# Optimization experiments

Measured on AMD Instinct MI355X. Metric: run time of the kernel, lower is better.

The kernel has to match this reference:

```python
import jax, jax.numpy as jnp
import numpy as np

N_NODES = 50000
N_EDGES = 800000
IN_CH = 128
HID = 32
HEADS = 8
OUT_CH = 40
NEG_SLOPE = 0.2


def setup_inputs() -> dict:
    key = jax.random.key(0)
    ks = jax.random.split(key, 12)
    g = lambda k, shape, fan: (jax.random.normal(k, shape, jnp.float32) / np.sqrt(fan).astype(np.float32))
    return {
        "x": jax.random.normal(ks[0], (N_NODES, IN_CH), jnp.float32),
        "edge_index": jax.random.randint(ks[1], (2, N_EDGES), 0, N_NODES, jnp.int64),
        "W1l": g(ks[2], (IN_CH, HEADS * HID), IN_CH),
        "W1r": g(ks[3], (IN_CH, HEADS * HID), IN_CH),
        "att1": g(ks[4], (HEADS, HID), HID),
        "b1": jnp.zeros((HEADS * HID,), jnp.float32),
        "W2l": g(ks[5], (HEADS * HID, HID), HEADS * HID),
        "W2r": g(ks[6], (HEADS * HID, HID), HEADS * HID),
        "att2": g(ks[7], (1, HID), HID),
        "b2": jnp.zeros((HID,), jnp.float32),
        "Wc": g(ks[8], (HID + IN_CH, OUT_CH), HID + IN_CH),
        "bc": jnp.zeros((OUT_CH,), jnp.float32),
    }


def _gatv2(x, ei, Wl, Wr, att, b, heads, ch):
    # GATv2Conv (concat=True): e_ij = att . LeakyReLU(Wl x_j + Wr x_i)
    n = x.shape[0]
    src, dst = ei[0], ei[1]  # message flows src(j) -> dst(i)
    xl = (x @ Wl).reshape(n, heads, ch)  # source transform
    xr = (x @ Wr).reshape(n, heads, ch)  # target transform
    e = jax.nn.leaky_relu(xl[src] + xr[dst], NEG_SLOPE)  # [E, H, C]
    score = jnp.einsum("ehc,hc->eh", e, att)             # [E, H]
    # per-target-node segment softmax (stable)
    m = jax.ops.segment_max(score, dst, num_segments=n)
    alpha = jnp.exp(score - m[dst])
    denom = jax.ops.segment_sum(alpha, dst, num_segments=n)
    alpha = alpha / denom[dst]
    out = jax.ops.segment_sum(alpha[:, :, None] * xl[src], dst, num_segments=n)
    return out.reshape(n, heads * ch) + b


def reference(x, edge_index, W1l, W1r, att1, b1, W2l, W2r, att2, b2, Wc, bc):
    n = x.shape[0]
    ar = jnp.arange(n, dtype=edge_index.dtype)
    ei = jnp.concatenate([edge_index, jnp.stack([ar, ar])], axis=1)  # add self-loops
    h1 = jax.nn.elu(_gatv2(x, ei, W1l, W1r, att1, b1, HEADS, HID))
    h2 = jax.nn.elu(_gatv2(h1, ei, W2l, W2r, att2, b2, 1, HID))
    combined = jnp.concatenate([h2, x], axis=1)
    return combined @ Wc + bc
```

## Files before the change

### kernel.cpp

```cpp
#include <hip/hip_runtime.h>
#include <cstdint>
#include <cstddef>
#include <math.h>

#define NN 50000
#define INCH 128
#define HIDC 32
#define NHEAD 8
#define OUTC 40

typedef unsigned short ushort_t;
using bf16x8 = __attribute__((ext_vector_type(8))) short;
using f32x4  = __attribute__((ext_vector_type(4))) float;

__device__ __forceinline__ float bf2f(unsigned short h) {
    return __uint_as_float(((unsigned int)h) << 16);
}
__device__ __forceinline__ unsigned short f2bf(float f) {
    unsigned int u = __float_as_uint(f);
    u = u + 0x7FFFu + ((u >> 16) & 1u);
    return (unsigned short)(u >> 16);
}
__device__ __forceinline__ float lo16(unsigned int u) { return __uint_as_float(u << 16); }
__device__ __forceinline__ float hi16(unsigned int u) { return __uint_as_float(u & 0xffff0000u); }

__global__ __launch_bounds__(256) void prep_all(
    const float* __restrict__ x, ushort_t* __restrict__ xb, int total8,
    const float* __restrict__ W1l, const float* __restrict__ W1r,
    const float* __restrict__ W2l, const float* __restrict__ W2r,
    const float* __restrict__ Wc,
    ushort_t* __restrict__ BT1, ushort_t* __restrict__ BT2, ushort_t* __restrict__ BTc,
    const int* __restrict__ ei, int E, int n, int* __restrict__ deg, int CX) {
    const int blk = blockIdx.x;
    const int tid = threadIdx.x;
    if (blk < CX) {
        int i = blk * 256 + tid;
        if (i >= total8) return;
        float4 f0 = *(const float4*)(x + (size_t)i * 8);
        float4 f1 = *(const float4*)(x + (size_t)i * 8 + 4);
        ushort4 u0, u1;
        u0.x = f2bf(f0.x); u0.y = f2bf(f0.y); u0.z = f2bf(f0.z); u0.w = f2bf(f0.w);
        u1.x = f2bf(f1.x); u1.y = f2bf(f1.y); u1.z = f2bf(f1.z); u1.w = f2bf(f1.w);
        *(ushort4*)(xb + (size_t)i * 8) = u0;
        *(ushort4*)(xb + (size_t)i * 8 + 4) = u1;
    } else if (blk < CX + 616) {
        int b = blk - CX, k = tid;
        if (b < 512) {
            if (k < 128) {
                float v = (b < 256) ? W1l[(size_t)k * 256 + b] : W1r[(size_t)k * 256 + (b - 256)];
                BT1[(size_t)b * 128 + k] = f2bf(v);
            }
        } else if (b < 576) {
            int c = b - 512;
            float v = (c < 32) ? W2l[(size_t)k * 32 + c] : W2r[(size_t)k * 32 + (c - 32)];
            BT2[(size_t)c * 256 + k] = f2bf(v);
        } else {
            int c = b - 576;
            if (k < 160) BTc[(size_t)c * 160 + k] = f2bf(Wc[(size_t)k * 40 + c]);
        }
    } else {
        int e = (blk - CX - 616) * 256 + tid;
        if (e >= E + n) return;
        int dst = (e < E) ? ei[E + e] : (e - E);
        atomicAdd(&deg[dst], 1);
    }
}


__global__ __launch_bounds__(1024) void partial_scan(
    const int* __restrict__ deg, int* __restrict__ row_start,
    int* __restrict__ block_total, int n) {
    __shared__ int wsum[16];
    const int tid = threadIdx.x, lane = tid & 63, wid = tid >> 6;
    int i = blockIdx.x * 1024 + tid;
    int v = (i < n) ? deg[i] : 0;
    int s = v;
    #pragma unroll
    for (int off = 1; off < 64; off <<= 1) {
        int t = __shfl_up(s, off, 64);
        if (lane >= off) s += t;
    }
    if (lane == 63) wsum[wid] = s;
    __syncthreads();
    if (wid == 0) {
        int ws = (lane < 16) ? wsum[lane] : 0;
        #pragma unroll
        for (int off = 1; off < 16; off <<= 1) {
            int t = __shfl_up(ws, off, 64);
            if (lane >= off) ws += t;
        }
        if (lane < 16) wsum[lane] = ws;
    }
    __syncthreads();
    int wexcl = wid ? wsum[wid - 1] : 0;
    if (i < n) row_start[i] = wexcl + s - v;
    if (tid == 0) block_total[blockIdx.x] = wsum[15];
}

__global__ void totals_scan(const int* __restrict__ block_total, int* __restrict__ block_off,
                            int* __restrict__ row_start_n, int nb) {
    int j = threadIdx.x;
    int v = (j < nb) ? block_total[j] : 0;
    int s = v;
    #pragma unroll
    for (int off = 1; off < 64; off <<= 1) {
        int t = __shfl_up(s, off, 64);
        if (j >= off) s += t;
    }
    if (j < nb) block_off[j] = s - v;
    if (j == nb - 1) *row_start_n = s;
}

__global__ __launch_bounds__(1024) void add_off(int* __restrict__ row_start, int* __restrict__ cursor,
                                                const int* __restrict__ block_off, int n) {
    int i = blockIdx.x * 1024 + threadIdx.x;
    if (i >= n) return;
    int val = row_start[i] + block_off[blockIdx.x];
    row_start[i] = val;
    cursor[i] = val;
}

__global__ void scatter_edges(const int* __restrict__ ei, int E, int n,
                              int* __restrict__ cursor, int* __restrict__ csr_src) {
    int e = blockIdx.x * blockDim.x + threadIdx.x;
    if (e >= E + n) return;
    int src, dst;
    if (e < E) { src = ei[e]; dst = ei[E + e]; } else { src = dst = e - E; }
    int pos = atomicAdd(&cursor[dst], 1);
    csr_src[pos] = src;
}

__global__ __launch_bounds__(256) void gemm1_mfma(
    const ushort_t* __restrict__ xb, const ushort_t* __restrict__ BT1,
    const float* __restrict__ att,
    ushort_t* __restrict__ xl1, ushort_t* __restrict__ xr1,
    float* __restrict__ dl, float* __restrict__ dr, int M) {
    __shared__ ushort_t As[128][72];
    __shared__ ushort_t Bs[128][72];
    const int tid = threadIdx.x;
    const int rowBase = blockIdx.y * 128;
    const int bx = blockIdx.x;
    const int c0 = bx * 128;
    const int wid = tid >> 6, lane = tid & 63;
    const int wr = wid >> 1, wc = wid & 1;
    const int l15 = lane & 15, l4 = lane >> 4;
    f32x4 acc[4][4];
    #pragma unroll
    for (int i = 0; i < 4; ++i)
        #pragma unroll
        for (int j = 0; j < 4; ++j)
            #pragma unroll
            for (int q = 0; q < 4; ++q) acc[i][j][q] = 0.f;

    for (int c = 0; c < 2; ++c) {
        #pragma unroll
        for (int h = 0; h < 4; ++h) {
            int idx = h * 256 + tid;
            int r = idx >> 3, seg = idx & 7;
            int row = rowBase + r;
            uint4 v = {0, 0, 0, 0};
            if (row < M) v = *(const uint4*)(xb + (size_t)row * 128 + c * 64 + seg * 8);
            *(uint4*)&As[r][seg * 8] = v;
            *(uint4*)&Bs[r][seg * 8] = *(const uint4*)(BT1 + (size_t)(c0 + r) * 128 + c * 64 + seg * 8);
        }
        __syncthreads();
        #pragma unroll
        for (int kk = 0; kk < 2; ++kk) {
            bf16x8 a[4], b[4];
            #pragma unroll
            for (int f = 0; f < 4; ++f) {
                a[f] = *(const bf16x8*)&As[wr * 64 + f * 16 + l15][kk * 32 + l4 * 8];
                b[f] = *(const bf16x8*)&Bs[wc * 64 + f * 16 + l15][kk * 32 + l4 * 8];
            }
            #pragma unroll
            for (int i = 0; i < 4; ++i)
                #pragma unroll
                for (int j = 0; j < 4; ++j)
                    acc[i][j] = __builtin_amdgcn_mfma_f32_16x16x32_bf16(a[i], b[j], acc[i][j], 0, 0, 0);
        }
        __syncthreads();
    }
    ushort_t* __restrict__ cout = (bx < 2) ? xl1 : xr1;
    const int colBase = (bx & 1) * 128;
    #pragma unroll
    for (int i = 0; i < 4; ++i)
        #pragma unroll
        for (int r = 0; r < 4; ++r) {
            int row = rowBase + wr * 64 + i * 16 + l4 * 4 + r;
            if (row >= M) continue;
            #pragma unroll
            for (int j = 0; j < 4; ++j) {
                int col = colBase + wc * 64 + j * 16 + l15;
                cout[(size_t)row * 256 + col] = f2bf(acc[i][j][r]);
            }
        }
    float attv[4];
    #pragma unroll
    for (int j = 0; j < 4; ++j)
        attv[j] = att[(bx & 1) * 128 + wc * 64 + j * 16 + l15];
    float* __restrict__ dst = (bx < 2) ? dl : dr;
    const int headA = (bx & 1) * 4 + wc * 2;
    #pragma unroll
    for (int i = 0; i < 4; ++i)
        #pragma unroll
        for (int r = 0; r < 4; ++r) {
            float s0 = fmaf(acc[i][1][r], attv[1], acc[i][0][r] * attv[0]);
            float s1 = fmaf(acc[i][3][r], attv[3], acc[i][2][r] * attv[2]);
            s0 += __shfl_xor(s0, 1); s1 += __shfl_xor(s1, 1);
            s0 += __shfl_xor(s0, 2); s1 += __shfl_xor(s1, 2);
            s0 += __shfl_xor(s0, 4); s1 += __shfl_xor(s1, 4);
            s0 += __shfl_xor(s0, 8); s1 += __shfl_xor(s1, 8);
            if (l15 == 0) {
                int row = rowBase + wr * 64 + i * 16 + l4 * 4 + r;
                if (row < M) {
                    dst[(size_t)row * 8 + headA] = s0;
                    dst[(size_t)row * 8 + headA + 1] = s1;
                }
            }
        }
}

__global__ __launch_bounds__(256) void gat_agg1(
    const ushort_t* __restrict__ xl, const ushort_t* __restrict__ xr,
    const float* __restrict__ dl, const float* __restrict__ dr,
    const float* __restrict__ att, const float* __restrict__ b,
    const int* __restrict__ row_start, const int* __restrict__ csr_src,
    ushort_t* __restrict__ h1) {
    const int lane = threadIdx.x & 63;
    const int i = blockIdx.x * 4 + (threadIdx.x >> 6);
    const int half = lane >> 5;
    const int sl = lane & 31;
    const int head = sl >> 2;

    uint4 xv = *(const uint4*)(xr + (size_t)i * 256 + sl * 8);
    const float xr0 = lo16(xv.x), xr1 = hi16(xv.x), xr2 = lo16(xv.y), xr3 = hi16(xv.y);
    const float xr4 = lo16(xv.z), xr5 = hi16(xv.z), xr6 = lo16(xv.w), xr7 = hi16(xv.w);
    const float4 atA = *(const float4*)(att + sl * 8);
    const float4 atB = *(const float4*)(att + sl * 8 + 4);
    const float cbase = 0.6f * dr[(size_t)i * 8 + head];
    const int p0 = row_start[i], p1 = row_start[i + 1];

    float d = 0.f;
    float a0 = 0.f, a1 = 0.f, a2 = 0.f, a3 = 0.f, a4 = 0.f, a5 = 0.f, a6 = 0.f, a7 = 0.f;

    int e0 = p0 + half;     int pc0 = e0 < p1 ? e0 : p1 - 1;
    int j0 = csr_src[pc0];
    uint4 uv0 = *(const uint4*)(xl + (size_t)j0 * 256 + sl * 8);
    float dl0 = dl[(size_t)j0 * 8 + head];
    int e1 = p0 + half + 2; int pc1 = e1 < p1 ? e1 : p1 - 1;
    int j1 = csr_src[pc1];
    uint4 uv1 = *(const uint4*)(xl + (size_t)j1 * 256 + sl * 8);
    float dl1 = dl[(size_t)j1 * 8 + head];

    for (int p = p0; p < p1; p += 4) {
        {
            const bool val = (p + half) < p1;
            float v0 = lo16(uv0.x), v1 = hi16(uv0.x), v2 = lo16(uv0.y), v3 = hi16(uv0.y);
            float v4 = lo16(uv0.z), v5 = hi16(uv0.z), v6 = lo16(uv0.w), v7 = hi16(uv0.w);
            float base = fmaf(0.6f, dl0, cbase);
            int nxt = p + half + 4;
            if (nxt < p1) {
                int jn = csr_src[nxt];
                uv0 = *(const uint4*)(xl + (size_t)jn * 256 + sl * 8);
                dl0 = dl[(size_t)jn * 8 + head];
            }
            float q = atA.x * fabsf(v0 + xr0);
            q = fmaf(atA.y, fabsf(v1 + xr1), q);
            q = fmaf(atA.z, fabsf(v2 + xr2), q);
            q = fmaf(atA.w, fabsf(v3 + xr3), q);
            q = fmaf(atB.x, fabsf(v4 + xr4), q);
            q = fmaf(atB.y, fabsf(v5 + xr5), q);
            q = fmaf(atB.z, fabsf(v6 + xr6), q);
            q = fmaf(atB.w, fabsf(v7 + xr7), q);
            q += __shfl_xor(q, 1);
            q += __shfl_xor(q, 2);
            float w = val ? __expf(fmaf(0.4f, q, base)) : 0.f;
            d += w;
            a0 = fmaf(w, v0, a0); a1 = fmaf(w, v1, a1);
            a2 = fmaf(w, v2, a2); a3 = fmaf(w, v3, a3);
            a4 = fmaf(w, v4, a4); a5 = fmaf(w, v5, a5);
            a6 = fmaf(w, v6, a6); a7 = fmaf(w, v7, a7);
        }
        {
            const bool val = (p + 2 + half) < p1;
            float v0 = lo16(uv1.x), v1 = hi16(uv1.x), v2 = lo16(uv1.y), v3 = hi16(uv1.y);
            float v4 = lo16(uv1.z), v5 = hi16(uv1.z), v6 = lo16(uv1.w), v7 = hi16(uv1.w);
            float base = fmaf(0.6f, dl1, cbase);
            int nxt = p + half + 6;
            if (nxt < p1) {
                int jn = csr_src[nxt];
                uv1 = *(const uint4*)(xl + (size_t)jn * 256 + sl * 8);
                dl1 = dl[(size_t)jn * 8 + head];
            }
            float q = atA.x * fabsf(v0 + xr0);
            q = fmaf(atA.y, fabsf(v1 + xr1), q);
            q = fmaf(atA.z, fabsf(v2 + xr2), q);
            q = fmaf(atA.w, fabsf(v3 + xr3), q);
            q = fmaf(atB.x, fabsf(v4 + xr4), q);
            q = fmaf(atB.y, fabsf(v5 + xr5), q);
            q = fmaf(atB.z, fabsf(v6 + xr6), q);
            q = fmaf(atB.w, fabsf(v7 + xr7), q);
            q += __shfl_xor(q, 1);
            q += __shfl_xor(q, 2);
            float w = val ? __expf(fmaf(0.4f, q, base)) : 0.f;
            d += w;
            a0 = fmaf(w, v0, a0); a1 = fmaf(w, v1, a1);
            a2 = fmaf(w, v2, a2); a3 = fmaf(w, v3, a3);
            a4 = fmaf(w, v4, a4); a5 = fmaf(w, v5, a5);
            a6 = fmaf(w, v6, a6); a7 = fmaf(w, v7, a7);
        }
    }
    d  += __shfl_xor(d, 32);
    a0 += __shfl_xor(a0, 32); a1 += __shfl_xor(a1, 32);
    a2 += __shfl_xor(a2, 32); a3 += __shfl_xor(a3, 32);
    a4 += __shfl_xor(a4, 32); a5 += __shfl_xor(a5, 32);
    a6 += __shfl_xor(a6, 32); a7 += __shfl_xor(a7, 32);

    if (half == 0) {
        const float4 bA = *(const float4*)(b + sl * 8);
        const float4 bB = *(const float4*)(b + sl * 8 + 4);
        float inv = 1.f / d;
        float o0 = fmaf(a0, inv, bA.x), o1 = fmaf(a1, inv, bA.y);
        float o2 = fmaf(a2, inv, bA.z), o3 = fmaf(a3, inv, bA.w);
        float o4 = fmaf(a4, inv, bB.x), o5 = fmaf(a5, inv, bB.y);
        float o6 = fmaf(a6, inv, bB.z), o7 = fmaf(a7, inv, bB.w);
        o0 = o0 > 0.f ? o0 : __expf(o0) - 1.f;
        o1 = o1 > 0.f ? o1 : __expf(o1) - 1.f;
        o2 = o2 > 0.f ? o2 : __expf(o2) - 1.f;
        o3 = o3 > 0.f ? o3 : __expf(o3) - 1.f;
        o4 = o4 > 0.f ? o4 : __expf(o4) - 1.f;
        o5 = o5 > 0.f ? o5 : __expf(o5) - 1.f;
        o6 = o6 > 0.f ? o6 : __expf(o6) - 1.f;
        o7 = o7 > 0.f ? o7 : __expf(o7) - 1.f;
        uint4 ov;
        ov.x = ((unsigned)f2bf(o1) << 16) | f2bf(o0);
        ov.y = ((unsigned)f2bf(o3) << 16) | f2bf(o2);
        ov.z = ((unsigned)f2bf(o5) << 16) | f2bf(o4);
        ov.w = ((unsigned)f2bf(o7) << 16) | f2bf(o6);
        *(uint4*)(h1 + (size_t)i * 256 + sl * 8) = ov;
    }
}

__global__ __launch_bounds__(256) void gemm2_mfma(
    const ushort_t* __restrict__ h1, const ushort_t* __restrict__ BT2,
    const float* __restrict__ att,
    ushort_t* __restrict__ xl2, ushort_t* __restrict__ xr2,
    float* __restrict__ dl2, float* __restrict__ dr2, int M) {
    __shared__ ushort_t As[128][72];
    __shared__ ushort_t Bs[64][264];
    const int tid = threadIdx.x;
    const int rowBase = blockIdx.x * 128;
    const int wid = tid >> 6, lane = tid & 63;
    const int l15 = lane & 15, l4 = lane >> 4;
    #pragma unroll
    for (int h = 0; h < 8; ++h) {
        int idx = h * 256 + tid;
        int r = idx >> 5, seg = idx & 31;
        *(uint4*)&Bs[r][seg * 8] = *(const uint4*)(BT2 + (size_t)r * 256 + seg * 8);
    }
    f32x4 acc[2][4];
    #pragma unroll
    for (int i = 0; i < 2; ++i)
        #pragma unroll
        for (int j = 0; j < 4; ++j)
            #pragma unroll
            for (int q = 0; q < 4; ++q) acc[i][j][q] = 0.f;

    for (int c = 0; c < 4; ++c) {
        #pragma unroll
        for (int h = 0; h < 4; ++h) {
            int idx = h * 256 + tid;
            int r = idx >> 3, seg = idx & 7;
            int row = rowBase + r;
            uint4 v = {0, 0, 0, 0};
            if (row < M) v = *(const uint4*)(h1 + (size_t)row * 256 + c * 64 + seg * 8);
            *(uint4*)&As[r][seg * 8] = v;
        }
        __syncthreads();
        #pragma unroll
        for (int kk = 0; kk < 2; ++kk) {
            bf16x8 a[2], b[4];
            #pragma unroll
            for (int f = 0; f < 2; ++f)
                a[f] = *(const bf16x8*)&As[wid * 32 + f * 16 + l15][kk * 32 + l4 * 8];
            #pragma unroll
            for (int f = 0; f < 4; ++f)
                b[f] = *(const bf16x8*)&Bs[f * 16 + l15][c * 64 + kk * 32 + l4 * 8];
            #pragma unroll
            for (int i = 0; i < 2; ++i)
                #pragma unroll
                for (int j = 0; j < 4; ++j)
                    acc[i][j] = __builtin_amdgcn_mfma_f32_16x16x32_bf16(a[i], b[j], acc[i][j], 0, 0, 0);
        }
        __syncthreads();
    }
    #pragma unroll
    for (int i = 0; i < 2; ++i)
        #pragma unroll
        for (int r = 0; r < 4; ++r) {
            int row = rowBase + wid * 32 + i * 16 + l4 * 4 + r;
            if (row >= M) continue;
            #pragma unroll
            for (int j = 0; j < 4; ++j) {
                int col = j * 16 + l15;
                if (col < 32) xl2[(size_t)row * 32 + col] = f2bf(acc[i][j][r]);
                else          xr2[(size_t)row * 32 + (col - 32)] = f2bf(acc[i][j][r]);
            }
        }
    float attv[4];
    #pragma unroll
    for (int j = 0; j < 4; ++j)
        attv[j] = att[(j * 16 + l15) & 31];
    #pragma unroll
    for (int i = 0; i < 2; ++i)
        #pragma unroll
        for (int r = 0; r < 4; ++r) {
            float s0 = fmaf(acc[i][1][r], attv[1], acc[i][0][r] * attv[0]);
            float s1 = fmaf(acc[i][3][r], attv[3], acc[i][2][r] * attv[2]);
            s0 += __shfl_xor(s0, 1); s1 += __shfl_xor(s1, 1);
            s0 += __shfl_xor(s0, 2); s1 += __shfl_xor(s1, 2);
            s0 += __shfl_xor(s0, 4); s1 += __shfl_xor(s1, 4);
            s0 += __shfl_xor(s0, 8); s1 += __shfl_xor(s1, 8);
            if (l15 == 0) {
                int row = rowBase + wid * 32 + i * 16 + l4 * 4 + r;
                if (row < M) {
                    dl2[row] = s0;
                    dr2[row] = s1;
                }
            }
        }
}

__global__ __launch_bounds__(256) void gat_agg2(
    const ushort_t* __restrict__ xl, const ushort_t* __restrict__ xr,
    const float* __restrict__ dl, const float* __restrict__ dr,
    const float* __restrict__ att, const float* __restrict__ b,
    const int* __restrict__ row_start, const int* __restrict__ csr_src,
    ushort_t* __restrict__ h2) {
    const int lane = threadIdx.x & 63;
    const int i = blockIdx.x * 4 + (threadIdx.x >> 6);
    const int g = lane >> 3;
    const int h8 = lane & 7;
    uint2 xv = *(const uint2*)(xr + (size_t)i * 32 + h8 * 4);
    const float xr0 = lo16(xv.x), xr1 = hi16(xv.x), xr2 = lo16(xv.y), xr3 = hi16(xv.y);
    const float4 at = *(const float4*)(att + h8 * 4);
    const float cbase = 0.6f * dr[i];
    const int p0 = row_start[i], p1 = row_start[i + 1];
    float d = 0.f, a0 = 0.f, a1 = 0.f, a2 = 0.f, a3 = 0.f;

    int e0 = p0 + g;     int pc0 = e0 < p1 ? e0 : p1 - 1;
    int j0 = csr_src[pc0];
    uint2 uv0 = *(const uint2*)(xl + (size_t)j0 * 32 + h8 * 4);
    float dl0 = dl[j0];
    int e1 = p0 + g + 8; int pc1 = e1 < p1 ? e1 : p1 - 1;
    int j1 = csr_src[pc1];
    uint2 uv1 = *(const uint2*)(xl + (size_t)j1 * 32 + h8 * 4);
    float dl1 = dl[j1];

    for (int p = p0; p < p1; p += 16) {
        {
            const bool val = (p + g) < p1;
            float v0 = lo16(uv0.x), v1 = hi16(uv0.x), v2 = lo16(uv0.y), v3 = hi16(uv0.y);
            float base = fmaf(0.6f, dl0, cbase);
            int nxt = p + g + 16;
            if (nxt < p1) {
                int jn = csr_src[nxt];
                uv0 = *(const uint2*)(xl + (size_t)jn * 32 + h8 * 4);
                dl0 = dl[jn];
            }
            float q = at.x * fabsf(v0 + xr0);
            q = fmaf(at.y, fabsf(v1 + xr1), q);
            q = fmaf(at.z, fabsf(v2 + xr2), q);
            q = fmaf(at.w, fabsf(v3 + xr3), q);
            q += __shfl_xor(q, 1);
            q += __shfl_xor(q, 2);
            q += __shfl_xor(q, 4);
            float w = val ? __expf(fmaf(0.4f, q, base)) : 0.f;
            d += w;
            a0 = fmaf(w, v0, a0); a1 = fmaf(w, v1, a1);
            a2 = fmaf(w, v2, a2); a3 = fmaf(w, v3, a3);
        }
        {
            const bool val = (p + g + 8) < p1;
            float v0 = lo16(uv1.x), v1 = hi16(uv1.x), v2 = lo16(uv1.y), v3 = hi16(uv1.y);
            float base = fmaf(0.6f, dl1, cbase);
            int nxt = p + g + 24;
            if (nxt < p1) {
                int jn = csr_src[nxt];
                uv1 = *(const uint2*)(xl + (size_t)jn * 32 + h8 * 4);
                dl1 = dl[jn];
            }
            float q = at.x * fabsf(v0 + xr0);
            q = fmaf(at.y, fabsf(v1 + xr1), q);
            q = fmaf(at.z, fabsf(v2 + xr2), q);
            q = fmaf(at.w, fabsf(v3 + xr3), q);
            q += __shfl_xor(q, 1);
            q += __shfl_xor(q, 2);
            q += __shfl_xor(q, 4);
            float w = val ? __expf(fmaf(0.4f, q, base)) : 0.f;
            d += w;
            a0 = fmaf(w, v0, a0); a1 = fmaf(w, v1, a1);
            a2 = fmaf(w, v2, a2); a3 = fmaf(w, v3, a3);
        }
    }
    d  += __shfl_xor(d, 8);  d  += __shfl_xor(d, 16);  d  += __shfl_xor(d, 32);
    a0 += __shfl_xor(a0, 8); a0 += __shfl_xor(a0, 16); a0 += __shfl_xor(a0, 32);
    a1 += __shfl_xor(a1, 8); a1 += __shfl_xor(a1, 16); a1 += __shfl_xor(a1, 32);
    a2 += __shfl_xor(a2, 8); a2 += __shfl_xor(a2, 16); a2 += __shfl_xor(a2, 32);
    a3 += __shfl_xor(a3, 8); a3 += __shfl_xor(a3, 16); a3 += __shfl_xor(a3, 32);
    if (g == 0) {
        const float4 bb = *(const float4*)(b + h8 * 4);
        float inv = 1.f / d;
        float o0 = fmaf(a0, inv, bb.x);
        float o1 = fmaf(a1, inv, bb.y);
        float o2 = fmaf(a2, inv, bb.z);
        float o3 = fmaf(a3, inv, bb.w);
        o0 = o0 > 0.f ? o0 : __expf(o0) - 1.f;
        o1 = o1 > 0.f ? o1 : __expf(o1) - 1.f;
        o2 = o2 > 0.f ? o2 : __expf(o2) - 1.f;
        o3 = o3 > 0.f ? o3 : __expf(o3) - 1.f;
        uint2 ov;
        ov.x = ((unsigned)f2bf(o1) << 16) | f2bf(o0);
        ov.y = ((unsigned)f2bf(o3) << 16) | f2bf(o2);
        *(uint2*)(h2 + (size_t)i * 32 + h8 * 4) = ov;
    }
}

__global__ __launch_bounds__(256) void final_mfma(
    const ushort_t* __restrict__ h2, const ushort_t* __restrict__ xb,
    const ushort_t* __restrict__ BTc, const float* __restrict__ bc,
    float* __restrict__ out, int M) {
    __shared__ ushort_t As[128][168];
    __shared__ ushort_t Bs[48][168];
    const int tid = threadIdx.x;
    const int rowBase = blockIdx.x * 128;
    const int wid = tid >> 6, lane = tid & 63;
    const int l15 = lane & 15, l4 = lane >> 4;
    #pragma unroll
    for (int h = 0; h < 4; ++h) {
        int idx = h * 256 + tid;
        if (idx < 960) {
            int r = idx / 20, seg = idx % 20;
            uint4 v = {0, 0, 0, 0};
            if (r < 40) v = *(const uint4*)(BTc + (size_t)r * 160 + seg * 8);
            *(uint4*)&Bs[r][seg * 8] = v;
        }
    }
    #pragma unroll
    for (int h = 0; h < 10; ++h) {
        int idx = h * 256 + tid;
        int r = idx / 20, seg = idx % 20;
        int row = rowBase + r;
        uint4 v = {0, 0, 0, 0};
        if (row < M)
            v = (seg < 4) ? *(const uint4*)(h2 + (size_t)row * 32 + seg * 8)
                          : *(const uint4*)(xb + (size_t)row * 128 + (seg - 4) * 8);
        *(uint4*)&As[r][seg * 8] = v;
    }
    __syncthreads();
    f32x4 acc[2][3];
    #pragma unroll
    for (int i = 0; i < 2; ++i)
        #pragma unroll
        for (int j = 0; j < 3; ++j)
            #pragma unroll
            for (int q = 0; q < 4; ++q) acc[i][j][q] = 0.f;
    #pragma unroll
    for (int kk = 0; kk < 5; ++kk) {
        bf16x8 a[2], b[3];
        #pragma unroll
        for (int f = 0; f < 2; ++f)
            a[f] = *(const bf16x8*)&As[wid * 32 + f * 16 + l15][kk * 32 + l4 * 8];
        #pragma unroll
        for (int f = 0; f < 3; ++f)
            b[f] = *(const bf16x8*)&Bs[f * 16 + l15][kk * 32 + l4 * 8];
        #pragma unroll
        for (int i = 0; i < 2; ++i)
            #pragma unroll
            for (int j = 0; j < 3; ++j)
                acc[i][j] = __builtin_amdgcn_mfma_f32_16x16x32_bf16(a[i], b[j], acc[i][j], 0, 0, 0);
    }
    #pragma unroll
    for (int i = 0; i < 2; ++i)
        #pragma unroll
        for (int r = 0; r < 4; ++r) {
            int row = rowBase + wid * 32 + i * 16 + l4 * 4 + r;
            if (row >= M) continue;
            #pragma unroll
            for (int j = 0; j < 3; ++j) {
                int col = j * 16 + l15;
                if (col < 40) out[(size_t)row * 40 + col] = acc[i][j][r] + bc[col];
            }
        }
}


extern "C" void kernel_launch(void* const* d_in, const int* in_sizes, int n_in,
                              void* d_out, int out_size, void* d_ws, size_t ws_size,
                              hipStream_t stream) {
    const float* x    = (const float*)d_in[0];
    const int*   ei   = (const int*)d_in[1];
    const float* W1l  = (const float*)d_in[2];
    const float* W1r  = (const float*)d_in[3];
    const float* att1 = (const float*)d_in[4];
    const float* b1   = (const float*)d_in[5];
    const float* W2l  = (const float*)d_in[6];
    const float* W2r  = (const float*)d_in[7];
    const float* att2 = (const float*)d_in[8];
    const float* b2   = (const float*)d_in[9];
    const float* Wc   = (const float*)d_in[10];
    const float* bc   = (const float*)d_in[11];
    float* out = (float*)d_out;

    const int n  = NN;
    const int E  = in_sizes[1] / 2;
    const int TE = E + n;
    const int NB = (n + 1023) / 1024;
    const int CX = (n * 128 / 8 + 255) / 256;
    const int CD = (TE + 255) / 256;

    char* ws = (char*)d_ws;
    size_t off = 0;
    auto alloc = [&](size_t bytes) { void* p = ws + off; off += (bytes + 255) & ~(size_t)255; return p; };
    ushort_t* xb   = (ushort_t*)alloc((size_t)n * 128 * 2);
    ushort_t* xl1  = (ushort_t*)alloc((size_t)n * 256 * 2);
    ushort_t* xr1  = (ushort_t*)alloc((size_t)n * 256 * 2);
    ushort_t* h1   = (ushort_t*)alloc((size_t)n * 256 * 2);
    ushort_t* xl2  = (ushort_t*)alloc((size_t)n * 32 * 2);
    ushort_t* xr2  = (ushort_t*)alloc((size_t)n * 32 * 2);
    ushort_t* h2   = (ushort_t*)alloc((size_t)n * 32 * 2);
    ushort_t* BT1  = (ushort_t*)alloc(512 * 128 * 2);
    ushort_t* BT2  = (ushort_t*)alloc(64 * 256 * 2);
    ushort_t* BTc  = (ushort_t*)alloc(40 * 160 * 2);
    float* dl1 = (float*)alloc((size_t)n * 8 * 4);
    float* dr1 = (float*)alloc((size_t)n * 8 * 4);
    float* dl2 = (float*)alloc((size_t)n * 4);
    float* dr2 = (float*)alloc((size_t)n * 4);
    int* row_start   = (int*)alloc((size_t)(n + 1) * 4);
    int* cursor      = (int*)alloc((size_t)(n + 1) * 4);
    int* deg         = (int*)alloc((size_t)n * 4);
    int* block_total = (int*)alloc((size_t)NB * 4);
    int* block_off   = (int*)alloc((size_t)NB * 4);
    int* csr_src     = (int*)alloc((size_t)TE * 4);

    hipMemsetAsync(deg, 0, (size_t)n * 4, stream);
    prep_all<<<CX + 616 + CD, 256, 0, stream>>>(x, xb, n * 128 / 8,
        W1l, W1r, W2l, W2r, Wc, BT1, BT2, BTc, ei, E, n, deg, CX);

    partial_scan<<<NB, 1024, 0, stream>>>(deg, row_start, block_total, n);
    totals_scan<<<1, 64, 0, stream>>>(block_total, block_off, row_start + n, NB);
    add_off<<<NB, 1024, 0, stream>>>(row_start, cursor, block_off, n);
    scatter_edges<<<CD, 256, 0, stream>>>(ei, E, n, cursor, csr_src);

    gemm1_mfma<<<dim3(4, (n + 127) / 128), 256, 0, stream>>>(xb, BT1, att1, xl1, xr1, dl1, dr1, n);
    gat_agg1<<<n / 4, 256, 0, stream>>>(xl1, xr1, dl1, dr1, att1, b1, row_start, csr_src, h1);

    gemm2_mfma<<<(n + 127) / 128, 256, 0, stream>>>(h1, BT2, att2, xl2, xr2, dl2, dr2, n);
    gat_agg2<<<n / 4, 256, 0, stream>>>(xl2, xr2, dl2, dr2, att2, b2, row_start, csr_src, h2);

    final_mfma<<<(n + 127) / 128, 256, 0, stream>>>(h2, xb, BTc, bc, out, n);
}
```

Baseline: 348.7 us.

## Merge scan kernels and use packed float2 math with peeled tails in aggregation

```diff
diff --git a/kernel.cpp b/kernel.cpp
--- a/kernel.cpp
+++ b/kernel.cpp
@@ -12,6 +12,7 @@
 typedef unsigned short ushort_t;
 using bf16x8 = __attribute__((ext_vector_type(8))) short;
 using f32x4  = __attribute__((ext_vector_type(4))) float;
+using f32x2  = __attribute__((ext_vector_type(2))) float;
 
 __device__ __forceinline__ float bf2f(unsigned short h) {
     return __uint_as_float(((unsigned int)h) << 16);
@@ -23,6 +24,12 @@
 }
 __device__ __forceinline__ float lo16(unsigned int u) { return __uint_as_float(u << 16); }
 __device__ __forceinline__ float hi16(unsigned int u) { return __uint_as_float(u & 0xffff0000u); }
+__device__ __forceinline__ f32x2 up2(unsigned int u) {
+    f32x2 r; r.x = lo16(u); r.y = hi16(u); return r;
+}
+__device__ __forceinline__ f32x2 pabs(f32x2 v) {
+    return __builtin_elementwise_max(v, -v);
+}
 
 __global__ __launch_bounds__(256) void prep_all(
     const float* __restrict__ x, ushort_t* __restrict__ xb, int total8,
@@ -97,27 +104,30 @@
     if (tid == 0) block_total[blockIdx.x] = wsum[15];
 }
 
-__global__ void totals_scan(const int* __restrict__ block_total, int* __restrict__ block_off,
-                            int* __restrict__ row_start_n, int nb) {
-    int j = threadIdx.x;
-    int v = (j < nb) ? block_total[j] : 0;
-    int s = v;
-    #pragma unroll
-    for (int off = 1; off < 64; off <<= 1) {
-        int t = __shfl_up(s, off, 64);
-        if (j >= off) s += t;
-    }
-    if (j < nb) block_off[j] = s - v;
-    if (j == nb - 1) *row_start_n = s;
-}
-
-__global__ __launch_bounds__(1024) void add_off(int* __restrict__ row_start, int* __restrict__ cursor,
-                                                const int* __restrict__ block_off, int n) {
+__global__ __launch_bounds__(1024) void scan_finish(
+    int* __restrict__ row_start, int* __restrict__ cursor,
+    const int* __restrict__ block_total, int n, int nb) {
+    __shared__ int s_off, s_tot;
+    if (threadIdx.x < 64) {
+        int j = threadIdx.x;
+        int v = (j < nb) ? block_total[j] : 0;
+        int off = (j < (int)blockIdx.x) ? v : 0;
+        int tot = v;
+        #pragma unroll
+        for (int o = 1; o < 64; o <<= 1) {
+            off += __shfl_xor(off, o);
+            tot += __shfl_xor(tot, o);
+        }
+        if (j == 0) { s_off = off; s_tot = tot; }
+    }
+    __syncthreads();
     int i = blockIdx.x * 1024 + threadIdx.x;
-    if (i >= n) return;
-    int val = row_start[i] + block_off[blockIdx.x];
-    row_start[i] = val;
-    cursor[i] = val;
+    if (i < n) {
+        int val = row_start[i] + s_off;
+        row_start[i] = val;
+        cursor[i] = val;
+    }
+    if (blockIdx.x == 0 && threadIdx.x == 0) row_start[n] = s_tot;
 }
 
 __global__ void scatter_edges(const int* __restrict__ ei, int E, int n,
@@ -233,97 +243,130 @@
     const int head = sl >> 2;
 
     uint4 xv = *(const uint4*)(xr + (size_t)i * 256 + sl * 8);
-    const float xr0 = lo16(xv.x), xr1 = hi16(xv.x), xr2 = lo16(xv.y), xr3 = hi16(xv.y);
-    const float xr4 = lo16(xv.z), xr5 = hi16(xv.z), xr6 = lo16(xv.w), xr7 = hi16(xv.w);
+    const f32x2 xr01 = up2(xv.x), xr23 = up2(xv.y), xr45 = up2(xv.z), xr67 = up2(xv.w);
     const float4 atA = *(const float4*)(att + sl * 8);
     const float4 atB = *(const float4*)(att + sl * 8 + 4);
+    f32x2 at01, at23, at45, at67;
+    at01.x = atA.x; at01.y = atA.y; at23.x = atA.z; at23.y = atA.w;
+    at45.x = atB.x; at45.y = atB.y; at67.x = atB.z; at67.y = atB.w;
     const float cbase = 0.6f * dr[(size_t)i * 8 + head];
     const int p0 = row_start[i], p1 = row_start[i + 1];
-
-    float d = 0.f;
-    float a0 = 0.f, a1 = 0.f, a2 = 0.f, a3 = 0.f, a4 = 0.f, a5 = 0.f, a6 = 0.f, a7 = 0.f;
-
-    int e0 = p0 + half;     int pc0 = e0 < p1 ? e0 : p1 - 1;
-    int j0 = csr_src[pc0];
-    uint4 uv0 = *(const uint4*)(xl + (size_t)j0 * 256 + sl * 8);
-    float dl0 = dl[(size_t)j0 * 8 + head];
-    int e1 = p0 + half + 2; int pc1 = e1 < p1 ? e1 : p1 - 1;
-    int j1 = csr_src[pc1];
-    uint4 uv1 = *(const uint4*)(xl + (size_t)j1 * 256 + sl * 8);
-    float dl1 = dl[(size_t)j1 * 8 + head];
-
-    for (int p = p0; p < p1; p += 4) {
+    const int deg = p1 - p0;
+    const int pfull = p0 + (deg & ~3);
+
+    float dsum = 0.f;
+    f32x2 a01 = {0.f, 0.f}, a23 = {0.f, 0.f}, a45 = {0.f, 0.f}, a67 = {0.f, 0.f};
+
+    int pcA = p0 + half;     pcA = pcA < p1 ? pcA : p1 - 1;
+    int jA = csr_src[pcA];
+    uint4 uvA = *(const uint4*)(xl + (size_t)jA * 256 + sl * 8);
+    float dlA = dl[(size_t)jA * 8 + head];
+    int pcB = p0 + 2 + half; pcB = pcB < p1 ? pcB : p1 - 1;
+    int jB = csr_src[pcB];
+    uint4 uvB = *(const uint4*)(xl + (size_t)jB * 256 + sl * 8);
+    float dlB = dl[(size_t)jB * 8 + head];
+
+    for (int p = p0; p < pfull; p += 4) {
         {
-            const bool val = (p + half) < p1;
-            float v0 = lo16(uv0.x), v1 = hi16(uv0.x), v2 = lo16(uv0.y), v3 = hi16(uv0.y);
-            float v4 = lo16(uv0.z), v5 = hi16(uv0.z), v6 = lo16(uv0.w), v7 = hi16(uv0.w);
-            float base = fmaf(0.6f, dl0, cbase);
-            int nxt = p + half + 4;
-            if (nxt < p1) {
-                int jn = csr_src[nxt];
-                uv0 = *(const uint4*)(xl + (size_t)jn * 256 + sl * 8);
-                dl0 = dl[(size_t)jn * 8 + head];
-            }
-            float q = atA.x * fabsf(v0 + xr0);
-            q = fmaf(atA.y, fabsf(v1 + xr1), q);
-            q = fmaf(atA.z, fabsf(v2 + xr2), q);
-            q = fmaf(atA.w, fabsf(v3 + xr3), q);
-            q = fmaf(atB.x, fabsf(v4 + xr4), q);
-            q = fmaf(atB.y, fabsf(v5 + xr5), q);
-            q = fmaf(atB.z, fabsf(v6 + xr6), q);
-            q = fmaf(atB.w, fabsf(v7 + xr7), q);
+            f32x2 v01 = up2(uvA.x), v23 = up2(uvA.y), v45 = up2(uvA.z), v67 = up2(uvA.w);
+            float base = fmaf(0.6f, dlA, cbase);
+            int nxt = p + 4 + half; int pc = nxt < p1 ? nxt : p1 - 1;
+            int jn = csr_src[pc];
+            uvA = *(const uint4*)(xl + (size_t)jn * 256 + sl * 8);
+            dlA = dl[(size_t)jn * 8 + head];
+            f32x2 q2 = at01 * pabs(v01 + xr01);
+            q2 = __builtin_elementwise_fma(at23, pabs(v23 + xr23), q2);
+            q2 = __builtin_elementwise_fma(at45, pabs(v45 + xr45), q2);
+            q2 = __builtin_elementwise_fma(at67, pabs(v67 + xr67), q2);
+            float q = q2.x + q2.y;
+            q += __shfl_xor(q, 1);
+            q += __shfl_xor(q, 2);
+            float w = __expf(fmaf(0.4f, q, base));
+            dsum += w;
+            f32x2 w2; w2.x = w; w2.y = w;
+            a01 = __builtin_elementwise_fma(w2, v01, a01);
+            a23 = __builtin_elementwise_fma(w2, v23, a23);
+            a45 = __builtin_elementwise_fma(w2, v45, a45);
+            a67 = __builtin_elementwise_fma(w2, v67, a67);
+        }
+        {
+            f32x2 v01 = up2(uvB.x), v23 = up2(uvB.y), v45 = up2(uvB.z), v67 = up2(uvB.w);
+            float base = fmaf(0.6f, dlB, cbase);
+            int nxt = p + 6 + half; int pc = nxt < p1 ? nxt : p1 - 1;
+            int jn = csr_src[pc];
+            uvB = *(const uint4*)(xl + (size_t)jn * 256 + sl * 8);
+            dlB = dl[(size_t)jn * 8 + head];
+            f32x2 q2 = at01 * pabs(v01 + xr01);
+            q2 = __builtin_elementwise_fma(at23, pabs(v23 + xr23), q2);
+            q2 = __builtin_elementwise_fma(at45, pabs(v45 + xr45), q2);
+            q2 = __builtin_elementwise_fma(at67, pabs(v67 + xr67), q2);
+            float q = q2.x + q2.y;
+            q += __shfl_xor(q, 1);
+            q += __shfl_xor(q, 2);
+            float w = __expf(fmaf(0.4f, q, base));
+            dsum += w;
+            f32x2 w2; w2.x = w; w2.y = w;
+            a01 = __builtin_elementwise_fma(w2, v01, a01);
+            a23 = __builtin_elementwise_fma(w2, v23, a23);
+            a45 = __builtin_elementwise_fma(w2, v45, a45);
+            a67 = __builtin_elementwise_fma(w2, v67, a67);
+        }
+    }
+    const int t = deg & 3;
+    if (t) {
+        {
+            const bool val = half < t;
+            f32x2 v01 = up2(uvA.x), v23 = up2(uvA.y), v45 = up2(uvA.z), v67 = up2(uvA.w);
+            float base = fmaf(0.6f, dlA, cbase);
+            f32x2 q2 = at01 * pabs(v01 + xr01);
+            q2 = __builtin_elementwise_fma(at23, pabs(v23 + xr23), q2);
+            q2 = __builtin_elementwise_fma(at45, pabs(v45 + xr45), q2);
+            q2 = __builtin_elementwise_fma(at67, pabs(v67 + xr67), q2);
+            float q = q2.x + q2.y;
             q += __shfl_xor(q, 1);
             q += __shfl_xor(q, 2);
             float w = val ? __expf(fmaf(0.4f, q, base)) : 0.f;
-            d += w;
-            a0 = fmaf(w, v0, a0); a1 = fmaf(w, v1, a1);
-            a2 = fmaf(w, v2, a2); a3 = fmaf(w, v3, a3);
-            a4 = fmaf(w, v4, a4); a5 = fmaf(w, v5, a5);
-            a6 = fmaf(w, v6, a6); a7 = fmaf(w, v7, a7);
-        }
-        {
-            const bool val = (p + 2 + half) < p1;
-            float v0 = lo16(uv1.x), v1 = hi16(uv1.x), v2 = lo16(uv1.y), v3 = hi16(uv1.y);
-            float v4 = lo16(uv1.z), v5 = hi16(uv1.z), v6 = lo16(uv1.w), v7 = hi16(uv1.w);
-            float base = fmaf(0.6f, dl1, cbase);
-            int nxt = p + half + 6;
-            if (nxt < p1) {
-                int jn = csr_src[nxt];
-                uv1 = *(const uint4*)(xl + (size_t)jn * 256 + sl * 8);
-                dl1 = dl[(size_t)jn * 8 + head];
-            }
-            float q = atA.x * fabsf(v0 + xr0);
-            q = fmaf(atA.y, fabsf(v1 + xr1), q);
-            q = fmaf(atA.z, fabsf(v2 + xr2), q);
-            q = fmaf(atA.w, fabsf(v3 + xr3), q);
-            q = fmaf(atB.x, fabsf(v4 + xr4), q);
-            q = fmaf(atB.y, fabsf(v5 + xr5), q);
-            q = fmaf(atB.z, fabsf(v6 + xr6), q);
-            q = fmaf(atB.w, fabsf(v7 + xr7), q);
+            dsum += w;
+            f32x2 w2; w2.x = w; w2.y = w;
+            a01 = __builtin_elementwise_fma(w2, v01, a01);
+            a23 = __builtin_elementwise_fma(w2, v23, a23);
+            a45 = __builtin_elementwise_fma(w2, v45, a45);
+            a67 = __builtin_elementwise_fma(w2, v67, a67);
+        }
+        if (t > 2) {
+            const bool val = (2 + half) < t;
+            f32x2 v01 = up2(uvB.x), v23 = up2(uvB.y), v45 = up2(uvB.z), v67 = up2(uvB.w);
+            float base = fmaf(0.6f, dlB, cbase);
+            f32x2 q2 = at01 * pabs(v01 + xr01);
+            q2 = __builtin_elementwise_fma(at23, pabs(v23 + xr23), q2);
+            q2 = __builtin_elementwise_fma(at45, pabs(v45 + xr45), q2);
+            q2 = __builtin_elementwise_fma(at67, pabs(v67 + xr67), q2);
+            float q = q2.x + q2.y;
             q += __shfl_xor(q, 1);
             q += __shfl_xor(q, 2);
             float w = val ? __expf(fmaf(0.4f, q, base)) : 0.f;
-            d += w;
-            a0 = fmaf(w, v0, a0); a1 = fmaf(w, v1, a1);
-            a2 = fmaf(w, v2, a2); a3 = fmaf(w, v3, a3);
-            a4 = fmaf(w, v4, a4); a5 = fmaf(w, v5, a5);
-            a6 = fmaf(w, v6, a6); a7 = fmaf(w, v7, a7);
-        }
-    }
-    d  += __shfl_xor(d, 32);
-    a0 += __shfl_xor(a0, 32); a1 += __shfl_xor(a1, 32);
-    a2 += __shfl_xor(a2, 32); a3 += __shfl_xor(a3, 32);
-    a4 += __shfl_xor(a4, 32); a5 += __shfl_xor(a5, 32);
-    a6 += __shfl_xor(a6, 32); a7 += __shfl_xor(a7, 32);
+            dsum += w;
+            f32x2 w2; w2.x = w; w2.y = w;
+            a01 = __builtin_elementwise_fma(w2, v01, a01);
+            a23 = __builtin_elementwise_fma(w2, v23, a23);
+            a45 = __builtin_elementwise_fma(w2, v45, a45);
+            a67 = __builtin_elementwise_fma(w2, v67, a67);
+        }
+    }
+    dsum += __shfl_xor(dsum, 32);
+    a01.x += __shfl_xor(a01.x, 32); a01.y += __shfl_xor(a01.y, 32);
+    a23.x += __shfl_xor(a23.x, 32); a23.y += __shfl_xor(a23.y, 32);
+    a45.x += __shfl_xor(a45.x, 32); a45.y += __shfl_xor(a45.y, 32);
+    a67.x += __shfl_xor(a67.x, 32); a67.y += __shfl_xor(a67.y, 32);
 
     if (half == 0) {
         const float4 bA = *(const float4*)(b + sl * 8);
         const float4 bB = *(const float4*)(b + sl * 8 + 4);
-        float inv = 1.f / d;
-        float o0 = fmaf(a0, inv, bA.x), o1 = fmaf(a1, inv, bA.y);
-        float o2 = fmaf(a2, inv, bA.z), o3 = fmaf(a3, inv, bA.w);
-        float o4 = fmaf(a4, inv, bB.x), o5 = fmaf(a5, inv, bB.y);
-        float o6 = fmaf(a6, inv, bB.z), o7 = fmaf(a7, inv, bB.w);
+        float inv = 1.f / dsum;
+        float o0 = fmaf(a01.x, inv, bA.x), o1 = fmaf(a01.y, inv, bA.y);
+        float o2 = fmaf(a23.x, inv, bA.z), o3 = fmaf(a23.y, inv, bA.w);
+        float o4 = fmaf(a45.x, inv, bB.x), o5 = fmaf(a45.y, inv, bB.y);
+        float o6 = fmaf(a67.x, inv, bB.z), o7 = fmaf(a67.y, inv, bB.w);
         o0 = o0 > 0.f ? o0 : __expf(o0) - 1.f;
         o1 = o1 > 0.f ? o1 : __expf(o1) - 1.f;
         o2 = o2 > 0.f ? o2 : __expf(o2) - 1.f;
@@ -442,79 +485,113 @@
     const int g = lane >> 3;
     const int h8 = lane & 7;
     uint2 xv = *(const uint2*)(xr + (size_t)i * 32 + h8 * 4);
-    const float xr0 = lo16(xv.x), xr1 = hi16(xv.x), xr2 = lo16(xv.y), xr3 = hi16(xv.y);
+    const f32x2 xr01 = up2(xv.x), xr23 = up2(xv.y);
     const float4 at = *(const float4*)(att + h8 * 4);
+    f32x2 at01, at23;
+    at01.x = at.x; at01.y = at.y; at23.x = at.z; at23.y = at.w;
     const float cbase = 0.6f * dr[i];
     const int p0 = row_start[i], p1 = row_start[i + 1];
-    float d = 0.f, a0 = 0.f, a1 = 0.f, a2 = 0.f, a3 = 0.f;
-
-    int e0 = p0 + g;     int pc0 = e0 < p1 ? e0 : p1 - 1;
-    int j0 = csr_src[pc0];
-    uint2 uv0 = *(const uint2*)(xl + (size_t)j0 * 32 + h8 * 4);
-    float dl0 = dl[j0];
-    int e1 = p0 + g + 8; int pc1 = e1 < p1 ? e1 : p1 - 1;
-    int j1 = csr_src[pc1];
-    uint2 uv1 = *(const uint2*)(xl + (size_t)j1 * 32 + h8 * 4);
-    float dl1 = dl[j1];
-
-    for (int p = p0; p < p1; p += 16) {
+    const int deg = p1 - p0;
+    const int pfull = p0 + (deg & ~15);
+    float dsum = 0.f;
+    f32x2 a01 = {0.f, 0.f}, a23 = {0.f, 0.f};
+
+    int pcA = p0 + g;     pcA = pcA < p1 ? pcA : p1 - 1;
+    int jA = csr_src[pcA];
+    uint2 uvA = *(const uint2*)(xl + (size_t)jA * 32 + h8 * 4);
+    float dlA = dl[jA];
+    int pcB = p0 + g + 8; pcB = pcB < p1 ? pcB : p1 - 1;
+    int jB = csr_src[pcB];
+    uint2 uvB = *(const uint2*)(xl + (size_t)jB * 32 + h8 * 4);
+    float dlB = dl[jB];
+
+    for (int p = p0; p < pfull; p += 16) {
         {
-            const bool val = (p + g) < p1;
-            float v0 = lo16(uv0.x), v1 = hi16(uv0.x), v2 = lo16(uv0.y), v3 = hi16(uv0.y);
-            float base = fmaf(0.6f, dl0, cbase);
-            int nxt = p + g + 16;
-            if (nxt < p1) {
-                int jn = csr_src[nxt];
-                uv0 = *(const uint2*)(xl + (size_t)jn * 32 + h8 * 4);
-                dl0 = dl[jn];
-            }
-            float q = at.x * fabsf(v0 + xr0);
-            q = fmaf(at.y, fabsf(v1 + xr1), q);
-            q = fmaf(at.z, fabsf(v2 + xr2), q);
-            q = fmaf(at.w, fabsf(v3 + xr3), q);
+            f32x2 v01 = up2(uvA.x), v23 = up2(uvA.y);
+            float base = fmaf(0.6f, dlA, cbase);
+            int nxt = p + g + 16; int pc = nxt < p1 ? nxt : p1 - 1;
+            int jn = csr_src[pc];
+            uvA = *(const uint2*)(xl + (size_t)jn * 32 + h8 * 4);
+            dlA = dl[jn];
+            f32x2 q2 = at01 * pabs(v01 + xr01);
+            q2 = __builtin_elementwise_fma(at23, pabs(v23 + xr23), q2);
+            float q = q2.x + q2.y;
+            q += __shfl_xor(q, 1);
+            q += __shfl_xor(q, 2);
+            q += __shfl_xor(q, 4);
+            float w = __expf(fmaf(0.4f, q, base));
+            dsum += w;
+            f32x2 w2; w2.x = w; w2.y = w;
+            a01 = __builtin_elementwise_fma(w2, v01, a01);
+            a23 = __builtin_elementwise_fma(w2, v23, a23);
+        }
+        {
+            f32x2 v01 = up2(uvB.x), v23 = up2(uvB.y);
+            float base = fmaf(0.6f, dlB, cbase);
+            int nxt = p + g + 24; int pc = nxt < p1 ? nxt : p1 - 1;
+            int jn = csr_src[pc];
+            uvB = *(const uint2*)(xl + (size_t)jn * 32 + h8 * 4);
+            dlB = dl[jn];
+            f32x2 q2 = at01 * pabs(v01 + xr01);
+            q2 = __builtin_elementwise_fma(at23, pabs(v23 + xr23), q2);
+            float q = q2.x + q2.y;
+            q += __shfl_xor(q, 1);
+            q += __shfl_xor(q, 2);
+            q += __shfl_xor(q, 4);
+            float w = __expf(fmaf(0.4f, q, base));
+            dsum += w;
+            f32x2 w2; w2.x = w; w2.y = w;
+            a01 = __builtin_elementwise_fma(w2, v01, a01);
+            a23 = __builtin_elementwise_fma(w2, v23, a23);
+        }
+    }
+    const int t = deg & 15;
+    if (t) {
+        {
+            const bool val = g < t;
+            f32x2 v01 = up2(uvA.x), v23 = up2(uvA.y);
+            float base = fmaf(0.6f, dlA, cbase);
+            f32x2 q2 = at01 * pabs(v01 + xr01);
+            q2 = __builtin_elementwise_fma(at23, pabs(v23 + xr23), q2);
+            float q = q2.x + q2.y;
             q += __shfl_xor(q, 1);
             q += __shfl_xor(q, 2);
             q += __shfl_xor(q, 4);
             float w = val ? __expf(fmaf(0.4f, q, base)) : 0.f;
-            d += w;
-            a0 = fmaf(w, v0, a0); a1 = fmaf(w, v1, a1);
-            a2 = fmaf(w, v2, a2); a3 = fmaf(w, v3, a3);
-        }
-        {
-            const bool val = (p + g + 8) < p1;
-            float v0 = lo16(uv1.x), v1 = hi16(uv1.x), v2 = lo16(uv1.y), v3 = hi16(uv1.y);
-            float base = fmaf(0.6f, dl1, cbase);
-            int nxt = p + g + 24;
-            if (nxt < p1) {
-                int jn = csr_src[nxt];
-                uv1 = *(const uint2*)(xl + (size_t)jn * 32 + h8 * 4);
-                dl1 = dl[jn];
-            }
-            float q = at.x * fabsf(v0 + xr0);
-            q = fmaf(at.y, fabsf(v1 + xr1), q);
-            q = fmaf(at.z, fabsf(v2 + xr2), q);
-            q = fmaf(at.w, fabsf(v3 + xr3), q);
+            dsum += w;
+            f32x2 w2; w2.x = w; w2.y = w;
+            a01 = __builtin_elementwise_fma(w2, v01, a01);
+            a23 = __builtin_elementwise_fma(w2, v23, a23);
+        }
+        if (t > 8) {
+            const bool val = (g + 8) < t;
+            f32x2 v01 = up2(uvB.x), v23 = up2(uvB.y);
+            float base = fmaf(0.6f, dlB, cbase);
+            f32x2 q2 = at01 * pabs(v01 + xr01);
+            q2 = __builtin_elementwise_fma(at23, pabs(v23 + xr23), q2);
+            float q = q2.x + q2.y;
             q += __shfl_xor(q, 1);
             q += __shfl_xor(q, 2);
             q += __shfl_xor(q, 4);
             float w = val ? __expf(fmaf(0.4f, q, base)) : 0.f;
-            d += w;
-            a0 = fmaf(w, v0, a0); a1 = fmaf(w, v1, a1);
-            a2 = fmaf(w, v2, a2); a3 = fmaf(w, v3, a3);
-        }
-    }
-    d  += __shfl_xor(d, 8);  d  += __shfl_xor(d, 16);  d  += __shfl_xor(d, 32);
-    a0 += __shfl_xor(a0, 8); a0 += __shfl_xor(a0, 16); a0 += __shfl_xor(a0, 32);
-    a1 += __shfl_xor(a1, 8); a1 += __shfl_xor(a1, 16); a1 += __shfl_xor(a1, 32);
-    a2 += __shfl_xor(a2, 8); a2 += __shfl_xor(a2, 16); a2 += __shfl_xor(a2, 32);
-    a3 += __shfl_xor(a3, 8); a3 += __shfl_xor(a3, 16); a3 += __shfl_xor(a3, 32);
+            dsum += w;
+            f32x2 w2; w2.x = w; w2.y = w;
+            a01 = __builtin_elementwise_fma(w2, v01, a01);
+            a23 = __builtin_elementwise_fma(w2, v23, a23);
+        }
+    }
+    dsum += __shfl_xor(dsum, 8);  dsum += __shfl_xor(dsum, 16);  dsum += __shfl_xor(dsum, 32);
+    a01.x += __shfl_xor(a01.x, 8); a01.x += __shfl_xor(a01.x, 16); a01.x += __shfl_xor(a01.x, 32);
+    a01.y += __shfl_xor(a01.y, 8); a01.y += __shfl_xor(a01.y, 16); a01.y += __shfl_xor(a01.y, 32);
+    a23.x += __shfl_xor(a23.x, 8); a23.x += __shfl_xor(a23.x, 16); a23.x += __shfl_xor(a23.x, 32);
+    a23.y += __shfl_xor(a23.y, 8); a23.y += __shfl_xor(a23.y, 16); a23.y += __shfl_xor(a23.y, 32);
     if (g == 0) {
         const float4 bb = *(const float4*)(b + h8 * 4);
-        float inv = 1.f / d;
-        float o0 = fmaf(a0, inv, bb.x);
-        float o1 = fmaf(a1, inv, bb.y);
-        float o2 = fmaf(a2, inv, bb.z);
-        float o3 = fmaf(a3, inv, bb.w);
+        float inv = 1.f / dsum;
+        float o0 = fmaf(a01.x, inv, bb.x);
+        float o1 = fmaf(a01.y, inv, bb.y);
+        float o2 = fmaf(a23.x, inv, bb.z);
+        float o3 = fmaf(a23.y, inv, bb.w);
         o0 = o0 > 0.f ? o0 : __expf(o0) - 1.f;
         o1 = o1 > 0.f ? o1 : __expf(o1) - 1.f;
         o2 = o2 > 0.f ? o2 : __expf(o2) - 1.f;
@@ -640,7 +717,6 @@
     int* cursor      = (int*)alloc((size_t)(n + 1) * 4);
     int* deg         = (int*)alloc((size_t)n * 4);
     int* block_total = (int*)alloc((size_t)NB * 4);
-    int* block_off   = (int*)alloc((size_t)NB * 4);
     int* csr_src     = (int*)alloc((size_t)TE * 4);
 
     hipMemsetAsync(deg, 0, (size_t)n * 4, stream);
@@ -648,8 +724,7 @@
         W1l, W1r, W2l, W2r, Wc, BT1, BT2, BTc, ei, E, n, deg, CX);
 
     partial_scan<<<NB, 1024, 0, stream>>>(deg, row_start, block_total, n);
-    totals_scan<<<1, 64, 0, stream>>>(block_total, block_off, row_start + n, NB);
-    add_off<<<NB, 1024, 0, stream>>>(row_start, cursor, block_off, n);
+    scan_finish<<<NB, 1024, 0, stream>>>(row_start, cursor, block_total, n, NB);
     scatter_edges<<<CD, 256, 0, stream>>>(ei, E, n, cursor, csr_src);
 
     gemm1_mfma<<<dim3(4, (n + 127) / 128), 256, 0, stream>>>(xb, BT1, att1, xl1, xr1, dl1, dr1, n);
```

Result: no change. 342.2 us (-1.9%).
